# Performance work log

Hardware: AMD Instinct MI355X
Metric: run time of the kernel (lower is better)

## Reference

```python
import jax, jax.numpy as jnp
import numpy as np

B, S, D, H, HD, W, DFF = 2, 8192, 768, 12, 64, 256, 3072
NEG = -1e9


def ln(x, s, b, eps):
    m = jnp.mean(x, axis=-1, keepdims=True)
    v = jnp.mean((x - m) ** 2, axis=-1, keepdims=True)
    return (x - m) / jnp.sqrt(v + eps) * s + b


def band_attn(q, k, v, w):
    # q,k,v: [B,H,S,HD]; q already scaled by 1/sqrt(HD).
    b, h, s, d = q.shape
    nc = s // w  # non-overlapping query chunks of size w
    qc = q.reshape(b, h, nc, w, d)
    pad = ((0, 0), (0, 0), (w, w), (0, 0))
    kp = jnp.pad(k, pad)
    vp = jnp.pad(v, pad)
    # key chunk c covers global positions [c*w - w, c*w + 2w) -> length 3w
    idx = jnp.arange(nc)[:, None] * w + jnp.arange(3 * w)[None, :]  # [nc,3w]
    kc = kp[:, :, idx]  # [B,H,nc,3w,HD]
    vc = vp[:, :, idx]
    scores = jnp.einsum('bhcqd,bhckd->bhcqk', qc, kc)  # [B,H,nc,w,3w]
    # relative offset key-query: key global = c*w - w + j, query global = c*w + i
    rel = jnp.arange(3 * w)[None, :] - w - jnp.arange(w)[:, None]  # [w,3w]
    band = jnp.abs(rel) <= w
    kpos = jnp.arange(nc)[:, None] * w - w + jnp.arange(3 * w)[None, :]  # [nc,3w]
    valid = (kpos >= 0) & (kpos < s)
    mask = band[None, :, :] & valid[:, None, :]  # [nc,w,3w]
    scores = jnp.where(mask, scores, NEG)
    probs = jax.nn.softmax(scores, axis=-1)
    out = jnp.einsum('bhcqk,bhckd->bhcqd', probs, vc)
    return out.reshape(b, h, s, d)


def longformer_layer(hidden, pos_emb, tt_emb, emb_ln_s, emb_ln_b,
                     wq, bq, wk, bk, wv, bv, wo, bo, attn_ln_s, attn_ln_b,
                     wi, bi, wo2, bo2, out_ln_s, out_ln_b):
    # embeddings: inputs_embeds + position + token_type(0), LN eps 1e-12
    h = ln(hidden + pos_emb[None, :hidden.shape[1]] + tt_emb, emb_ln_s, emb_ln_b, 1e-12)
    def heads(x):
        return x.reshape(B, S, H, HD).transpose(0, 2, 1, 3)
    q = heads(h @ wq + bq) / jnp.sqrt(jnp.float32(HD))
    k = heads(h @ wk + bk)
    v = heads(h @ wv + bv)
    a = band_attn(q, k, v, W)  # [B,H,S,HD]
    a = a.transpose(0, 2, 1, 3).reshape(B, S, D)
    h2 = ln(h + (a @ wo + bo), attn_ln_s, attn_ln_b, 1e-12)
    inter = jax.nn.gelu(h2 @ wi + bi, approximate=False)
    return ln(h2 + (inter @ wo2 + bo2), out_ln_s, out_ln_b, 1e-12)


def setup_inputs() -> dict:
    key = jax.random.key(0)
    ks = jax.random.split(key, 16)
    wn = lambda k, shp: jax.random.normal(k, shp, jnp.float32) * 0.02
    d = {
        'src': jax.random.normal(ks[0], (B, S, D), jnp.float32),
        'pos_emb': wn(ks[1], (S, D)),
        'tt_emb': wn(ks[2], (D,)),
        'emb_ln_s': jnp.ones((D,)), 'emb_ln_b': jnp.zeros((D,)),
        'wq': wn(ks[3], (D, D)), 'bq': jnp.zeros((D,)),
        'wk': wn(ks[4], (D, D)), 'bk': jnp.zeros((D,)),
        'wv': wn(ks[5], (D, D)), 'bv': jnp.zeros((D,)),
        'wo': wn(ks[6], (D, D)), 'bo': jnp.zeros((D,)),
        'attn_ln_s': jnp.ones((D,)), 'attn_ln_b': jnp.zeros((D,)),
        'wi': wn(ks[7], (D, DFF)), 'bi': jnp.zeros((DFF,)),
        'wo2': wn(ks[8], (DFF, D)), 'bo2': jnp.zeros((D,)),
        'out_ln_s': jnp.ones((D,)), 'out_ln_b': jnp.zeros((D,)),
        'n1_s': jnp.ones((D,)), 'n1_b': jnp.zeros((D,)),
        'n2_s': jnp.ones((D,)), 'n2_b': jnp.zeros((D,)),
        'w1': wn(ks[9], (D, DFF)), 'b1': jnp.zeros((DFF,)),
        'w2': wn(ks[10], (DFF, D)), 'b2': jnp.zeros((D,)),
    }
    return d


def reference(src, pos_emb, tt_emb, emb_ln_s, emb_ln_b, wq, bq, wk, bk, wv, bv,
              wo, bo, attn_ln_s, attn_ln_b, wi, bi, wo2, bo2, out_ln_s, out_ln_b,
              n1_s, n1_b, n2_s, n2_b, w1, b1, w2, b2):
    hidden = ln(src, n1_s, n1_b, 1e-5)
    out = longformer_layer(hidden, pos_emb, tt_emb, emb_ln_s, emb_ln_b,
                           wq, bq, wk, bk, wv, bv, wo, bo, attn_ln_s, attn_ln_b,
                           wi, bi, wo2, bo2, out_ln_s, out_ln_b)
    src2 = src + out  # dropout is identity in eval
    ff = jax.nn.relu(ln(src2, n2_s, n2_b, 1e-5) @ w1 + b1)
    ff = ff @ w2 + b2
    return src2 + ff
```

## Files before the change

kernel.cpp:

```cpp
#include <hip/hip_runtime.h>

#define SLEN 8192
#define BD   768
#define NH   12
#define NTOK 16384
#define HTOK 8192

typedef __bf16 bf16;
typedef __bf16 bf16x8 __attribute__((ext_vector_type(8)));
typedef float  floatx4 __attribute__((ext_vector_type(4)));

#define MFMA16(a, b, c) __builtin_amdgcn_mfma_f32_16x16x32_bf16((a), (b), (c), 0, 0, 0)

__device__ __forceinline__ int iclamp(int v, int lo, int hi) {
  return v < lo ? lo : (v > hi ? hi : v);
}

__device__ __forceinline__ void gl2lds16(const bf16* g, bf16* l) {
  __builtin_amdgcn_global_load_lds(
      (const __attribute__((address_space(1))) void*)g,
      (__attribute__((address_space(3))) void*)l,
      16, 0, 0);
}

__global__ __launch_bounds__(256) void k_prep_w(const float* __restrict__ W,
                                                bf16* __restrict__ Wt,
                                                int K, int N, float scale) {
  __shared__ float tile[32][33];
  const int tid = threadIdx.x;
  const int tx = tid & 31, ty = tid >> 5;
  const int n0 = blockIdx.x * 32, k0 = blockIdx.y * 32;
#pragma unroll
  for (int i = 0; i < 32; i += 8)
    tile[ty + i][tx] = W[(size_t)(k0 + ty + i) * N + n0 + tx];
  __syncthreads();
#pragma unroll
  for (int i = 0; i < 32; i += 8)
    Wt[(size_t)(n0 + ty + i) * K + k0 + tx] = (bf16)(tile[tx][ty + i] * scale);
}

__global__ void k_prep_qkv_bias(const float* __restrict__ bq, const float* __restrict__ bk,
                                const float* __restrict__ bv, float* __restrict__ out) {
  int i = blockIdx.x * 256 + threadIdx.x;
  if (i < 768) out[i] = bq[i] * 0.125f;
  else if (i < 1536) out[i] = bk[i - 768];
  else if (i < 2304) out[i] = bv[i - 1536];
}

__device__ __forceinline__ float block_sum768(float v, float* red) {
#pragma unroll
  for (int off = 32; off > 0; off >>= 1) v += __shfl_down(v, off);
  __syncthreads();
  if ((threadIdx.x & 63) == 0) red[threadIdx.x >> 6] = v;
  __syncthreads();
  return red[0] + red[1] + red[2] + red[3];
}

__global__ __launch_bounds__(256) void k_ln_ln_emb(const float* __restrict__ src,
    const float* __restrict__ pos, const float* __restrict__ tt,
    const float* __restrict__ s1, const float* __restrict__ b1,
    const float* __restrict__ s2, const float* __restrict__ b2,
    float* __restrict__ hf, bf16* __restrict__ hb) {
  __shared__ float red[4];
  const int tid = threadIdx.x;
  const size_t row = blockIdx.x;
  const int sp = blockIdx.x & (SLEN - 1);
  const float* x = src + row * BD;
  float v0 = x[tid], v1 = x[tid + 256], v2 = x[tid + 512];
  const float mean = block_sum768(v0 + v1 + v2, red) * (1.f / 768.f);
  v0 -= mean; v1 -= mean; v2 -= mean;
  const float var = block_sum768(v0 * v0 + v1 * v1 + v2 * v2, red) * (1.f / 768.f);
  const float rstd = rsqrtf(var + 1e-5f);
  const float* pr = pos + (size_t)sp * BD;
  float y0 = v0 * rstd * s1[tid]       + b1[tid]       + pr[tid]       + tt[tid];
  float y1 = v1 * rstd * s1[tid + 256] + b1[tid + 256] + pr[tid + 256] + tt[tid + 256];
  float y2 = v2 * rstd * s1[tid + 512] + b1[tid + 512] + pr[tid + 512] + tt[tid + 512];
  const float mean2 = block_sum768(y0 + y1 + y2, red) * (1.f / 768.f);
  y0 -= mean2; y1 -= mean2; y2 -= mean2;
  const float var2 = block_sum768(y0 * y0 + y1 * y1 + y2 * y2, red) * (1.f / 768.f);
  const float rstd2 = rsqrtf(var2 + 1e-12f);
  float o0 = y0 * rstd2 * s2[tid]       + b2[tid];
  float o1 = y1 * rstd2 * s2[tid + 256] + b2[tid + 256];
  float o2 = y2 * rstd2 * s2[tid + 512] + b2[tid + 512];
  float* hr = hf + row * BD;
  bf16* hbr = hb + row * BD;
  hr[tid] = o0; hr[tid + 256] = o1; hr[tid + 512] = o2;
  hbr[tid] = (bf16)o0; hbr[tid + 256] = (bf16)o1; hbr[tid + 512] = (bf16)o2;
}

__global__ __launch_bounds__(256) void k_ln(const float* __restrict__ x,
    const float* __restrict__ s, const float* __restrict__ b, float eps,
    float* __restrict__ of, bf16* __restrict__ ob) {
  __shared__ float red[4];
  const int tid = threadIdx.x;
  const size_t row = blockIdx.x;
  const float* xr = x + row * BD;
  float v0 = xr[tid], v1 = xr[tid + 256], v2 = xr[tid + 512];
  const float mean = block_sum768(v0 + v1 + v2, red) * (1.f / 768.f);
  v0 -= mean; v1 -= mean; v2 -= mean;
  const float var = block_sum768(v0 * v0 + v1 * v1 + v2 * v2, red) * (1.f / 768.f);
  const float rstd = rsqrtf(var + eps);
  float o0 = v0 * rstd * s[tid] + b[tid];
  float o1 = v1 * rstd * s[tid + 256] + b[tid + 256];
  float o2 = v2 * rstd * s[tid + 512] + b[tid + 512];
  float* ofr = of + row * BD; bf16* obr = ob + row * BD;
  ofr[tid] = o0; ofr[tid + 256] = o1; ofr[tid + 512] = o2;
  obr[tid] = (bf16)o0; obr[tid + 256] = (bf16)o1; obr[tid + 512] = (bf16)o2;
}

__global__ __launch_bounds__(256) void k_ln_add_ln(const float* __restrict__ y,
    const float* __restrict__ src,
    const float* __restrict__ so, const float* __restrict__ bo_,
    const float* __restrict__ s2, const float* __restrict__ b2,
    float* __restrict__ src2, bf16* __restrict__ tb) {
  __shared__ float red[4];
  const int tid = threadIdx.x;
  const size_t row = blockIdx.x;
  const float* xr = y + row * BD;
  float v0 = xr[tid], v1 = xr[tid + 256], v2 = xr[tid + 512];
  const float mean = block_sum768(v0 + v1 + v2, red) * (1.f / 768.f);
  v0 -= mean; v1 -= mean; v2 -= mean;
  const float var = block_sum768(v0 * v0 + v1 * v1 + v2 * v2, red) * (1.f / 768.f);
  const float rstd = rsqrtf(var + 1e-12f);
  const float* sr = src + row * BD;
  float u0 = sr[tid]       + v0 * rstd * so[tid]       + bo_[tid];
  float u1 = sr[tid + 256] + v1 * rstd * so[tid + 256] + bo_[tid + 256];
  float u2 = sr[tid + 512] + v2 * rstd * so[tid + 512] + bo_[tid + 512];
  float* s2r = src2 + row * BD;
  s2r[tid] = u0; s2r[tid + 256] = u1; s2r[tid + 512] = u2;
  const float mean2 = block_sum768(u0 + u1 + u2, red) * (1.f / 768.f);
  u0 -= mean2; u1 -= mean2; u2 -= mean2;
  const float var2 = block_sum768(u0 * u0 + u1 * u1 + u2 * u2, red) * (1.f / 768.f);
  const float rstd2 = rsqrtf(var2 + 1e-5f);
  bf16* tr = tb + row * BD;
  tr[tid]       = (bf16)(u0 * rstd2 * s2[tid]       + b2[tid]);
  tr[tid + 256] = (bf16)(u1 * rstd2 * s2[tid + 256] + b2[tid + 256]);
  tr[tid + 512] = (bf16)(u2 * rstd2 * s2[tid + 512] + b2[tid + 512]);
}

template <int ACT, bool RES, bool OUTB>
__global__ __launch_bounds__(256, 4) void k_gemm(const bf16* __restrict__ A,
                                                 const bf16* __restrict__ Bt,
                                                 const float* __restrict__ bias,
                                                 const float* __restrict__ resid,
                                                 float* __restrict__ Cf,
                                                 bf16* __restrict__ Cb,
                                                 int M, int N, int K) {
  __shared__ __align__(16) bf16 As[2][128 * 32];
  __shared__ __align__(16) bf16 Bs[2][128 * 32];
  const int tid = threadIdx.x;
  const int lane = tid & 63, wave = tid >> 6;
  const int quad = lane >> 4, c = lane & 15;
  const int wr = wave >> 1, wc = wave & 1;
  const int n0 = blockIdx.x * 128, m0 = blockIdx.y * 128;

  const int rA0 = wave * 32 + (lane >> 2);
  const int rA1 = rA0 + 16;
  const int gch = (((lane & 3) ^ ((lane >> 3) & 3)) << 3);
  const bf16* gA0 = A  + (size_t)(m0 + rA0) * K + gch;
  const bf16* gA1 = A  + (size_t)(m0 + rA1) * K + gch;
  const bf16* gB0 = Bt + (size_t)(n0 + rA0) * K + gch;
  const bf16* gB1 = Bt + (size_t)(n0 + rA1) * K + gch;
  const int ldst = wave * 1024;

  const int xorq = ((quad ^ ((c >> 1) & 3)) << 3);
  int aOff[4], bOff[4];
#pragma unroll
  for (int i = 0; i < 4; ++i) {
    aOff[i] = (wr * 64 + i * 16 + c) * 32 + xorq;
    bOff[i] = (wc * 64 + i * 16 + c) * 32 + xorq;
  }

  floatx4 acc[4][4];
#pragma unroll
  for (int i = 0; i < 4; ++i)
#pragma unroll
    for (int j = 0; j < 4; ++j) acc[i][j] = floatx4{0.f, 0.f, 0.f, 0.f};

  auto stage = [&](int buf, int k0) {
    gl2lds16(gA0 + k0, &As[buf][ldst]);
    gl2lds16(gA1 + k0, &As[buf][ldst + 512]);
    gl2lds16(gB0 + k0, &Bs[buf][ldst]);
    gl2lds16(gB1 + k0, &Bs[buf][ldst + 512]);
  };

  stage(0, 0);
  int cur = 0;
  for (int k0 = 0; k0 < K; k0 += 32) {
    __syncthreads();
    if (k0 + 32 < K) stage(cur ^ 1, k0 + 32);
    bf16x8 af[4], bfv[4];
#pragma unroll
    for (int i = 0; i < 4; ++i) af[i] = *(const bf16x8*)(&As[cur][aOff[i]]);
#pragma unroll
    for (int j = 0; j < 4; ++j) bfv[j] = *(const bf16x8*)(&Bs[cur][bOff[j]]);
#pragma unroll
    for (int i = 0; i < 4; ++i)
#pragma unroll
      for (int j = 0; j < 4; ++j)
        acc[i][j] = MFMA16(af[i], bfv[j], acc[i][j]);
    cur ^= 1;
  }

  const int rbase = m0 + wr * 64 + quad * 4;
  const int cbase = n0 + wc * 64 + c;
#pragma unroll
  for (int i = 0; i < 4; ++i) {
#pragma unroll
    for (int j = 0; j < 4; ++j) {
      const int col = cbase + j * 16;
      const float bc = bias[col];
#pragma unroll
      for (int r = 0; r < 4; ++r) {
        const int row = rbase + i * 16 + r;
        float v = acc[i][j][r] + bc;
        if (RES) v += resid[(size_t)row * N + col];
        if (ACT == 1) v = 0.5f * v * (1.f + erff(v * 0.70710678118654752f));
        if (ACT == 2) v = fmaxf(v, 0.f);
        if (OUTB) Cb[(size_t)row * N + col] = (bf16)v;
        else      Cf[(size_t)row * N + col] = v;
      }
    }
  }
}

__global__ __launch_bounds__(256) void k_vtrans(const bf16* __restrict__ qkv_b, bf16* __restrict__ vt) {
  __shared__ bf16 tile[64][72];
  const int tid = threadIdx.x;
  const int blk = blockIdx.x;
  const int h  = blk >> 7;
  const int st = blk & 127;
  const int s0 = st * 64;
  {
    const int d = tid & 63, si4 = tid >> 6;
    const bf16* src = qkv_b + (size_t)s0 * 2304 + 1536 + h * 64 + d;
#pragma unroll
    for (int i = 0; i < 16; ++i) {
      int s = si4 * 16 + i;
      tile[s][d] = src[(size_t)s * 2304];
    }
  }
  __syncthreads();
  {
    const int s = tid & 63, di4 = tid >> 6;
#pragma unroll
    for (int i = 0; i < 16; ++i) {
      int d = di4 * 16 + i;
      vt[((size_t)(h * 64 + d)) * SLEN + s0 + s] = tile[s][d];
    }
  }
}

__global__ __launch_bounds__(256, 4) void k_attn(const bf16* __restrict__ qkv_b,
                                                 const bf16* __restrict__ vt,
                                                 bf16* __restrict__ aout_b) {
  __shared__ __align__(16) bf16 Ks[2][64 * 64];
  __shared__ __align__(16) bf16 Vs[2][64 * 64];
  __shared__ __align__(16) bf16 Ps[4][16 * 64];
  const int tid  = threadIdx.x;
  const int wave = tid >> 6, lane = tid & 63;
  const int quad = lane >> 4, c = lane & 15;
  const int blk0 = blockIdx.x;
  const int wg   = ((blk0 & 7) * 192) + (blk0 >> 3);
  const int h    = wg >> 7;
  const int st   = wg & 127;
  const int q0b  = st * 64;
  const int q0   = q0b + wave * 16;

  const bf16* qp = qkv_b + (size_t)(q0 + c) * 2304 + h * 64 + quad * 8;
  const bf16x8 aq0 = *(const bf16x8*)(qp);
  const bf16x8 aq1 = *(const bf16x8*)(qp + 32);

  const int srow  = lane >> 3;
  const int chunk = ((lane & 7) ^ srow) << 3;
  const int krow0 = wave * 16 + srow;

  const int xlo = (quad ^ (c & 7)) << 3;
  const int xhi = ((quad + 4) ^ (c & 7)) << 3;

  floatx4 o[4];
  float m[4], l[4];
#pragma unroll
  for (int r = 0; r < 4; ++r) {
    o[r] = floatx4{0.f, 0.f, 0.f, 0.f};
    m[r] = -1e30f; l[r] = 0.f;
  }
  bf16* Pw = &Ps[wave][0];

  const int t_lo = st < 4 ? 4 - st : 0;
  const int t_hi = st > 123 ? 132 - st : 9;

  auto stage = [&](int buf, int t) {
    const int kb  = q0b - 256 + 64 * t;
    const int kr0 = iclamp(kb + krow0, 0, SLEN - 1);
    const int kr1 = iclamp(kb + krow0 + 8, 0, SLEN - 1);
    gl2lds16(qkv_b + (size_t)kr0 * 2304 + 768 + h * 64 + chunk, &Ks[buf][wave * 1024]);
    gl2lds16(qkv_b + (size_t)kr1 * 2304 + 768 + h * 64 + chunk, &Ks[buf][wave * 1024 + 512]);
    const int kbc = iclamp(kb, 0, SLEN - 64);
    gl2lds16(vt + (size_t)(h * 64 + krow0) * SLEN + kbc + chunk, &Vs[buf][wave * 1024]);
    gl2lds16(vt + (size_t)(h * 64 + krow0 + 8) * SLEN + kbc + chunk, &Vs[buf][wave * 1024 + 512]);
  };

  int cur = 0;
  stage(0, t_lo);
  for (int t = t_lo; t < t_hi; ++t) {
    __syncthreads();
    if (t + 1 < t_hi) stage(cur ^ 1, t + 1);
    const int kb = q0b - 256 + 64 * t;
    const bf16* Kb = &Ks[cur][0];
    const bf16* Vb = &Vs[cur][0];

    floatx4 s[4];
#pragma unroll
    for (int i = 0; i < 4; ++i) s[i] = floatx4{0.f, 0.f, 0.f, 0.f};
#pragma unroll
    for (int ks = 0; ks < 4; ++ks) {
      const bf16* kr = Kb + (ks * 16 + c) * 64;
      s[ks] = MFMA16(aq0, *(const bf16x8*)(kr + xlo), s[ks]);
      s[ks] = MFMA16(aq1, *(const bf16x8*)(kr + xhi), s[ks]);
    }
    if (t == 0 || t == 8) {
#pragma unroll
      for (int ks = 0; ks < 4; ++ks)
#pragma unroll
        for (int r = 0; r < 4; ++r) {
          int d = (kb + ks * 16 + c) - (q0 + quad * 4 + r);
          d = d < 0 ? -d : d;
          if (d > 256) s[ks][r] = -INFINITY;
        }
    }

    float tm[4], rs[4];
#pragma unroll
    for (int r = 0; r < 4; ++r)
      tm[r] = fmaxf(fmaxf(s[0][r], s[1][r]), fmaxf(s[2][r], s[3][r]));
#pragma unroll
    for (int off = 1; off < 16; off <<= 1)
#pragma unroll
      for (int r = 0; r < 4; ++r) tm[r] = fmaxf(tm[r], __shfl_xor(tm[r], off));
#pragma unroll
    for (int r = 0; r < 4; ++r) {
      const float mn = fmaxf(m[r], tm[r]);
      const float al = __expf(m[r] - mn);
      m[r] = mn;
      float sum = 0.f;
#pragma unroll
      for (int ks = 0; ks < 4; ++ks) { s[ks][r] = __expf(s[ks][r] - mn); sum += s[ks][r]; }
      rs[r] = sum;
      l[r] *= al;
#pragma unroll
      for (int n = 0; n < 4; ++n) o[n][r] *= al;
    }
#pragma unroll
    for (int off = 1; off < 16; off <<= 1)
#pragma unroll
      for (int r = 0; r < 4; ++r) rs[r] += __shfl_xor(rs[r], off);
#pragma unroll
    for (int r = 0; r < 4; ++r) l[r] += rs[r];

#pragma unroll
    for (int ks = 0; ks < 4; ++ks)
#pragma unroll
      for (int r = 0; r < 4; ++r) {
        const int prow = quad * 4 + r;
        const int col  = ks * 16 + c;
        Pw[prow * 64 + ((((col >> 3) ^ (prow & 7)) << 3) | (col & 7))] = (bf16)s[ks][r];
      }
    asm volatile("s_waitcnt lgkmcnt(0)" ::: "memory");
    const bf16x8 pa0 = *(const bf16x8*)(Pw + c * 64 + xlo);
    const bf16x8 pa1 = *(const bf16x8*)(Pw + c * 64 + xhi);
#pragma unroll
    for (int n = 0; n < 4; ++n) {
      const bf16* vr = Vb + (n * 16 + c) * 64;
      o[n] = MFMA16(pa0, *(const bf16x8*)(vr + xlo), o[n]);
      o[n] = MFMA16(pa1, *(const bf16x8*)(vr + xhi), o[n]);
    }
    cur ^= 1;
  }

#pragma unroll
  for (int r = 0; r < 4; ++r) {
    const float inv = 1.f / l[r];
    const size_t orow = (size_t)(q0 + quad * 4 + r) * BD + h * 64;
#pragma unroll
    for (int n = 0; n < 4; ++n)
      aout_b[orow + n * 16 + c] = (bf16)(o[n][r] * inv);
  }
}

extern "C" void kernel_launch(void* const* d_in, const int* in_sizes, int n_in,
                              void* d_out, int out_size, void* d_ws, size_t ws_size,
                              hipStream_t stream) {
  (void)in_sizes; (void)n_in; (void)out_size; (void)ws_size;
  const float* src     = (const float*)d_in[0];
  const float* pos_emb = (const float*)d_in[1];
  const float* tt_emb  = (const float*)d_in[2];
  const float* emb_s   = (const float*)d_in[3];
  const float* emb_b   = (const float*)d_in[4];
  const float* wq      = (const float*)d_in[5];
  const float* bq      = (const float*)d_in[6];
  const float* wk      = (const float*)d_in[7];
  const float* bk      = (const float*)d_in[8];
  const float* wv      = (const float*)d_in[9];
  const float* bv      = (const float*)d_in[10];
  const float* wo      = (const float*)d_in[11];
  const float* bo      = (const float*)d_in[12];
  const float* atn_s   = (const float*)d_in[13];
  const float* atn_b   = (const float*)d_in[14];
  const float* wi      = (const float*)d_in[15];
  const float* bi      = (const float*)d_in[16];
  const float* wo2     = (const float*)d_in[17];
  const float* bo2     = (const float*)d_in[18];
  const float* out_s   = (const float*)d_in[19];
  const float* out_b   = (const float*)d_in[20];
  const float* n1_s    = (const float*)d_in[21];
  const float* n1_b    = (const float*)d_in[22];
  const float* n2_s    = (const float*)d_in[23];
  const float* n2_b    = (const float*)d_in[24];
  const float* w1      = (const float*)d_in[25];
  const float* b1      = (const float*)d_in[26];
  const float* w2      = (const float*)d_in[27];
  const float* b2      = (const float*)d_in[28];

  char* ws = (char*)d_ws;
  size_t off = 0;
  auto alloc = [&](size_t bytes) {
    char* p = ws + off;
    off += (bytes + 255) & ~(size_t)255;
    return p;
  };

  bf16* qkvt  = (bf16*)alloc((size_t)2304 * 768 * 2);
  bf16* wot   = (bf16*)alloc((size_t)768 * 768 * 2);
  bf16* wit   = (bf16*)alloc((size_t)3072 * 768 * 2);
  bf16* wo2t  = (bf16*)alloc((size_t)768 * 3072 * 2);
  bf16* w1t   = (bf16*)alloc((size_t)3072 * 768 * 2);
  bf16* w2t   = (bf16*)alloc((size_t)768 * 3072 * 2);
  float* qkvb = (float*)alloc((size_t)2304 * 4);
  char* R1 = alloc((size_t)NTOK * BD * 4);
  char* R2 = alloc((size_t)NTOK * BD * 2);
  char* R3 = alloc((size_t)HTOK * 2304 * 2
                 + (size_t)NH * 64 * SLEN * 2
                 + (size_t)HTOK * BD * 2);

  float* h_f   = (float*)R1;
  bf16*  hb    = (bf16*)R2;
  bf16*  qkvB  = (bf16*)R3;
  bf16*  vtB   = (bf16*)(R3 + (size_t)HTOK * 2304 * 2);
  bf16*  aoutB = (bf16*)(R3 + (size_t)HTOK * 2304 * 2 + (size_t)NH * 64 * SLEN * 2);
  float* y1    = (float*)d_out;
  float* h2f   = (float*)R1;
  bf16*  h2b   = (bf16*)R2;
  bf16*  interC= (bf16*)R3;
  float* y2    = (float*)d_out;
  float* src2  = (float*)R1;
  bf16*  tb    = (bf16*)R2;
  bf16*  ff1C  = (bf16*)R3;
  float* outp  = (float*)d_out;

  dim3 blk(256);
  k_prep_w<<<dim3(24, 24), blk, 0, stream>>>(wq, qkvt,                 768, 768, 0.125f);
  k_prep_w<<<dim3(24, 24), blk, 0, stream>>>(wk, qkvt + 768 * 768,     768, 768, 1.f);
  k_prep_w<<<dim3(24, 24), blk, 0, stream>>>(wv, qkvt + 2 * 768 * 768, 768, 768, 1.f);
  k_prep_w<<<dim3(24, 24), blk, 0, stream>>>(wo, wot,                  768, 768, 1.f);
  k_prep_w<<<dim3(96, 24), blk, 0, stream>>>(wi, wit,    768, 3072, 1.f);
  k_prep_w<<<dim3(24, 96), blk, 0, stream>>>(wo2, wo2t, 3072, 768,  1.f);
  k_prep_w<<<dim3(96, 24), blk, 0, stream>>>(w1, w1t,    768, 3072, 1.f);
  k_prep_w<<<dim3(24, 96), blk, 0, stream>>>(w2, w2t,   3072, 768,  1.f);
  k_prep_qkv_bias<<<dim3(9), blk, 0, stream>>>(bq, bk, bv, qkvb);

  k_ln_ln_emb<<<dim3(NTOK), blk, 0, stream>>>(src, pos_emb, tt_emb, n1_s, n1_b,
                                              emb_s, emb_b, h_f, hb);
  for (int b = 0; b < 2; ++b) {
    const size_t tok0 = (size_t)b * HTOK;
    k_gemm<0, false, true><<<dim3(18, 64), blk, 0, stream>>>(
        hb + tok0 * BD, qkvt, qkvb, nullptr, nullptr, qkvB, HTOK, 2304, 768);
    k_vtrans<<<dim3(NH * 128), blk, 0, stream>>>(qkvB, vtB);
    k_attn<<<dim3(NH * 128), blk, 0, stream>>>(qkvB, vtB, aoutB);
    k_gemm<0, true, false><<<dim3(6, 64), blk, 0, stream>>>(
        aoutB, wot, bo, h_f + tok0 * BD, y1 + tok0 * BD, nullptr, HTOK, 768, 768);
  }
  k_ln<<<dim3(NTOK), blk, 0, stream>>>(y1, atn_s, atn_b, 1e-12f, h2f, h2b);
  for (int cchunk = 0; cchunk < 2; ++cchunk) {
    const size_t tok0 = (size_t)cchunk * HTOK;
    k_gemm<1, false, true><<<dim3(24, 64), blk, 0, stream>>>(
        h2b + tok0 * BD, wit, bi, nullptr, nullptr, interC, HTOK, 3072, 768);
    k_gemm<0, true, false><<<dim3(6, 64), blk, 0, stream>>>(
        interC, wo2t, bo2, h2f + tok0 * BD, y2 + tok0 * BD, nullptr, HTOK, 768, 3072);
  }
  k_ln_add_ln<<<dim3(NTOK), blk, 0, stream>>>(y2, src, out_s, out_b, n2_s, n2_b, src2, tb);
  for (int cchunk = 0; cchunk < 2; ++cchunk) {
    const size_t tok0 = (size_t)cchunk * HTOK;
    k_gemm<2, false, true><<<dim3(24, 64), blk, 0, stream>>>(
        tb + tok0 * BD, w1t, b1, nullptr, nullptr, ff1C, HTOK, 3072, 768);
    k_gemm<0, true, false><<<dim3(6, 64), blk, 0, stream>>>(
        ff1C, w2t, b2, src2 + tok0 * BD, outp + tok0 * BD, nullptr, HTOK, 768, 3072);
  }
}
```

Baseline: 1.085 ms.

## Add 64-row GEMM tile variant, XCD-aware block remap, and per-shape occupancy bounds

The GEMM kernel now takes the M tile size and min-waves launch bound as template parameters. The N=768 output projections use a 64x128 tile, which doubles the block count so more CUs are busy on these narrow GEMMs. The wide GEMMs keep 128x128 tiles but lower the occupancy hint to 2. Block IDs are remapped so consecutive tiles land on the same XCD for L2 locality. Smaller tiles cut per-block reuse of B, and the remap assumes the grid size divides by 8.

```diff
diff --git a/kernel.cpp b/kernel.cpp
--- a/kernel.cpp
+++ b/kernel.cpp
@@ -138,50 +138,65 @@
   tr[tid + 512] = (bf16)(u2 * rstd2 * s2[tid + 512] + b2[tid + 512]);
 }
 
-template <int ACT, bool RES, bool OUTB>
-__global__ __launch_bounds__(256, 4) void k_gemm(const bf16* __restrict__ A,
-                                                 const bf16* __restrict__ Bt,
-                                                 const float* __restrict__ bias,
-                                                 const float* __restrict__ resid,
-                                                 float* __restrict__ Cf,
-                                                 bf16* __restrict__ Cb,
-                                                 int M, int N, int K) {
-  __shared__ __align__(16) bf16 As[2][128 * 32];
+template <int BM, int MINW, int ACT, bool RES, bool OUTB>
+__global__ __launch_bounds__(256, MINW) void k_gemm(const bf16* __restrict__ A,
+                                                    const bf16* __restrict__ Bt,
+                                                    const float* __restrict__ bias,
+                                                    const float* __restrict__ resid,
+                                                    float* __restrict__ Cf,
+                                                    bf16* __restrict__ Cb,
+                                                    int M, int N, int K) {
+  __shared__ __align__(16) bf16 As[2][BM * 32];
   __shared__ __align__(16) bf16 Bs[2][128 * 32];
+  constexpr int NJ = (BM == 128) ? 4 : 2;
   const int tid = threadIdx.x;
   const int lane = tid & 63, wave = tid >> 6;
   const int quad = lane >> 4, c = lane & 15;
-  const int wr = wave >> 1, wc = wave & 1;
-  const int n0 = blockIdx.x * 128, m0 = blockIdx.y * 128;
-
-  const int rA0 = wave * 32 + (lane >> 2);
-  const int rA1 = rA0 + 16;
-  const int gch = (((lane & 3) ^ ((lane >> 3) & 3)) << 3);
-  const bf16* gA0 = A  + (size_t)(m0 + rA0) * K + gch;
-  const bf16* gA1 = A  + (size_t)(m0 + rA1) * K + gch;
-  const bf16* gB0 = Bt + (size_t)(n0 + rA0) * K + gch;
-  const bf16* gB1 = Bt + (size_t)(n0 + rA1) * K + gch;
-  const int ldst = wave * 1024;
+  const int gx = gridDim.x;
+  const int G  = gx * gridDim.y;
+  const int bid = blockIdx.y * gx + blockIdx.x;
+  const int wgid = (bid & 7) * (G >> 3) + (bid >> 3);
+  const int bx = wgid % gx, by = wgid / gx;
+  const int n0 = bx * 128, m0 = by * BM;
+
+  const int wrb = (BM == 128) ? (wave >> 1) * 64 : 0;
+  const int wcb = (BM == 128) ? (wave & 1) * 64 : wave * 32;
+
+  const int srow = lane >> 2;
+  const int gch  = (((lane & 3) ^ ((lane >> 3) & 3)) << 3);
+  const bf16* gA0;
+  const bf16* gA1 = nullptr;
+  int ldsA0, ldsA1 = 0;
+  if constexpr (BM == 128) {
+    gA0 = A + (size_t)(m0 + wave * 32 + srow) * K + gch;
+    gA1 = A + (size_t)(m0 + wave * 32 + 16 + srow) * K + gch;
+    ldsA0 = wave * 1024; ldsA1 = wave * 1024 + 512;
+  } else {
+    gA0 = A + (size_t)(m0 + wave * 16 + srow) * K + gch;
+    ldsA0 = wave * 512;
+  }
+  const bf16* gB0 = Bt + (size_t)(n0 + wave * 32 + srow) * K + gch;
+  const bf16* gB1 = Bt + (size_t)(n0 + wave * 32 + 16 + srow) * K + gch;
+  const int ldsB0 = wave * 1024, ldsB1 = wave * 1024 + 512;
 
   const int xorq = ((quad ^ ((c >> 1) & 3)) << 3);
-  int aOff[4], bOff[4];
-#pragma unroll
-  for (int i = 0; i < 4; ++i) {
-    aOff[i] = (wr * 64 + i * 16 + c) * 32 + xorq;
-    bOff[i] = (wc * 64 + i * 16 + c) * 32 + xorq;
-  }
-
-  floatx4 acc[4][4];
+  int aOff[4], bOff[NJ];
+#pragma unroll
+  for (int i = 0; i < 4; ++i) aOff[i] = (wrb + i * 16 + c) * 32 + xorq;
+#pragma unroll
+  for (int j = 0; j < NJ; ++j) bOff[j] = (wcb + j * 16 + c) * 32 + xorq;
+
+  floatx4 acc[4][NJ];
 #pragma unroll
   for (int i = 0; i < 4; ++i)
 #pragma unroll
-    for (int j = 0; j < 4; ++j) acc[i][j] = floatx4{0.f, 0.f, 0.f, 0.f};
+    for (int j = 0; j < NJ; ++j) acc[i][j] = floatx4{0.f, 0.f, 0.f, 0.f};
 
   auto stage = [&](int buf, int k0) {
-    gl2lds16(gA0 + k0, &As[buf][ldst]);
-    gl2lds16(gA1 + k0, &As[buf][ldst + 512]);
-    gl2lds16(gB0 + k0, &Bs[buf][ldst]);
-    gl2lds16(gB1 + k0, &Bs[buf][ldst + 512]);
+    gl2lds16(gA0 + k0, &As[buf][ldsA0]);
+    if constexpr (BM == 128) gl2lds16(gA1 + k0, &As[buf][ldsA1]);
+    gl2lds16(gB0 + k0, &Bs[buf][ldsB0]);
+    gl2lds16(gB1 + k0, &Bs[buf][ldsB1]);
   };
 
   stage(0, 0);
@@ -189,25 +204,25 @@
   for (int k0 = 0; k0 < K; k0 += 32) {
     __syncthreads();
     if (k0 + 32 < K) stage(cur ^ 1, k0 + 32);
-    bf16x8 af[4], bfv[4];
+    bf16x8 af[4], bfv[NJ];
 #pragma unroll
     for (int i = 0; i < 4; ++i) af[i] = *(const bf16x8*)(&As[cur][aOff[i]]);
 #pragma unroll
-    for (int j = 0; j < 4; ++j) bfv[j] = *(const bf16x8*)(&Bs[cur][bOff[j]]);
+    for (int j = 0; j < NJ; ++j) bfv[j] = *(const bf16x8*)(&Bs[cur][bOff[j]]);
 #pragma unroll
     for (int i = 0; i < 4; ++i)
 #pragma unroll
-      for (int j = 0; j < 4; ++j)
+      for (int j = 0; j < NJ; ++j)
         acc[i][j] = MFMA16(af[i], bfv[j], acc[i][j]);
     cur ^= 1;
   }
 
-  const int rbase = m0 + wr * 64 + quad * 4;
-  const int cbase = n0 + wc * 64 + c;
+  const int rbase = m0 + wrb + quad * 4;
+  const int cbase = n0 + wcb + c;
 #pragma unroll
   for (int i = 0; i < 4; ++i) {
 #pragma unroll
-    for (int j = 0; j < 4; ++j) {
+    for (int j = 0; j < NJ; ++j) {
       const int col = cbase + j * 16;
       const float bc = bias[col];
 #pragma unroll
@@ -222,6 +237,7 @@
       }
     }
   }
+  (void)M;
 }
 
 __global__ __launch_bounds__(256) void k_vtrans(const bf16* __restrict__ qkv_b, bf16* __restrict__ vt) {
@@ -473,27 +489,27 @@
                                               emb_s, emb_b, h_f, hb);
   for (int b = 0; b < 2; ++b) {
     const size_t tok0 = (size_t)b * HTOK;
-    k_gemm<0, false, true><<<dim3(18, 64), blk, 0, stream>>>(
+    k_gemm<128, 2, 0, false, true><<<dim3(18, 64), blk, 0, stream>>>(
         hb + tok0 * BD, qkvt, qkvb, nullptr, nullptr, qkvB, HTOK, 2304, 768);
     k_vtrans<<<dim3(NH * 128), blk, 0, stream>>>(qkvB, vtB);
     k_attn<<<dim3(NH * 128), blk, 0, stream>>>(qkvB, vtB, aoutB);
-    k_gemm<0, true, false><<<dim3(6, 64), blk, 0, stream>>>(
+    k_gemm<64, 4, 0, true, false><<<dim3(6, 128), blk, 0, stream>>>(
         aoutB, wot, bo, h_f + tok0 * BD, y1 + tok0 * BD, nullptr, HTOK, 768, 768);
   }
   k_ln<<<dim3(NTOK), blk, 0, stream>>>(y1, atn_s, atn_b, 1e-12f, h2f, h2b);
   for (int cchunk = 0; cchunk < 2; ++cchunk) {
     const size_t tok0 = (size_t)cchunk * HTOK;
-    k_gemm<1, false, true><<<dim3(24, 64), blk, 0, stream>>>(
+    k_gemm<128, 2, 1, false, true><<<dim3(24, 64), blk, 0, stream>>>(
         h2b + tok0 * BD, wit, bi, nullptr, nullptr, interC, HTOK, 3072, 768);
-    k_gemm<0, true, false><<<dim3(6, 64), blk, 0, stream>>>(
+    k_gemm<64, 4, 0, true, false><<<dim3(6, 128), blk, 0, stream>>>(
         interC, wo2t, bo2, h2f + tok0 * BD, y2 + tok0 * BD, nullptr, HTOK, 768, 3072);
   }
   k_ln_add_ln<<<dim3(NTOK), blk, 0, stream>>>(y2, src, out_s, out_b, n2_s, n2_b, src2, tb);
   for (int cchunk = 0; cchunk < 2; ++cchunk) {
     const size_t tok0 = (size_t)cchunk * HTOK;
-    k_gemm<2, false, true><<<dim3(24, 64), blk, 0, stream>>>(
+    k_gemm<128, 2, 2, false, true><<<dim3(24, 64), blk, 0, stream>>>(
         tb + tok0 * BD, w1t, b1, nullptr, nullptr, ff1C, HTOK, 3072, 768);
-    k_gemm<0, true, false><<<dim3(6, 64), blk, 0, stream>>>(
+    k_gemm<64, 4, 0, true, false><<<dim3(6, 128), blk, 0, stream>>>(
         ff1C, w2t, b2, src2 + tok0 * BD, outp + tok0 * BD, nullptr, HTOK, 768, 3072);
   }
 }
```

Result: faster. 1.052 ms (-3.1%).
